# Performance work log

Measured on AMD Instinct MI355X. Metric: run time of the kernel, lower is better.

The kernel has to match this reference:

```python
import jax, jax.numpy as jnp
import numpy as np

B, S, H = 32, 2048, 1024
UNITS = 1024


def setup_inputs() -> dict:
    key = jax.random.key(0)
    ks = jax.random.split(key, 8)
    scale_h = 1.0 / np.sqrt(H)
    scale_u = 1.0 / np.sqrt(UNITS)
    return {
        "query": jax.random.normal(ks[0], (B, H), dtype=jnp.float32),
        "values": jax.random.normal(ks[1], (B, S, H), dtype=jnp.float32),
        "W1": jax.random.normal(ks[2], (H, UNITS), dtype=jnp.float32) * scale_h,
        "b1": jnp.zeros((UNITS,), dtype=jnp.float32),
        "W2": jax.random.normal(ks[3], (H, UNITS), dtype=jnp.float32) * scale_h,
        "b2": jnp.zeros((UNITS,), dtype=jnp.float32),
        "V": jax.random.normal(ks[4], (UNITS, 1), dtype=jnp.float32) * scale_u,
        "bv": jnp.zeros((1,), dtype=jnp.float32),
    }


def reference(query, values, W1, b1, W2, b2, V, bv):
    # proj_v: [B, S, units]; proj_q: [B, 1, units] (query expanded on time axis)
    proj_v = jnp.einsum("bsh,hu->bsu", values, W1) + b1
    proj_q = (query @ W2 + b2)[:, None, :]
    # score: [B, S, 1]
    score = jnp.tanh(proj_v + proj_q) @ V + bv
    attention_weights = jax.nn.softmax(score, axis=1)  # softmax over seq axis
    context_vector = jnp.sum(attention_weights * values, axis=1)  # [B, H]
    return context_vector, attention_weights
```

## Files before the change

### kernel.cpp

```cpp
#include <hip/hip_runtime.h>

#define H 1024
#define UNITS 1024
#define BATCH 32
#define SEQ 2048
#define M_TOT (BATCH * SEQ)

typedef __attribute__((ext_vector_type(8))) short bf16x8;
typedef __attribute__((ext_vector_type(8))) unsigned short u16x8;
typedef __attribute__((ext_vector_type(4))) float f32x4;

__device__ __forceinline__ unsigned short f2bf(float f) {
  union { float f; unsigned u; } x; x.f = f;
  unsigned r = x.u + 0x7FFFu + ((x.u >> 16) & 1u);
  return (unsigned short)(r >> 16);
}
__device__ __forceinline__ float bf2f(unsigned short h) {
  union { unsigned u; float f; } x; x.u = (unsigned)h << 16;
  return x.f;
}

__device__ __forceinline__ void gll16(const unsigned short* g, unsigned short* l) {
  __builtin_amdgcn_global_load_lds(
      (const __attribute__((address_space(1))) void*)g,
      (__attribute__((address_space(3))) void*)l, 16, 0, 0);
}

__global__ void k_cast(const float* __restrict__ in, unsigned short* __restrict__ out) {
  size_t i = ((size_t)blockIdx.x * 256 + threadIdx.x) * 8;
  float4 v0 = *reinterpret_cast<const float4*>(in + i);
  float4 v1 = *reinterpret_cast<const float4*>(in + i + 4);
  union { unsigned short h[8]; u16x8 v; } p;
  p.h[0] = f2bf(v0.x); p.h[1] = f2bf(v0.y); p.h[2] = f2bf(v0.z); p.h[3] = f2bf(v0.w);
  p.h[4] = f2bf(v1.x); p.h[5] = f2bf(v1.y); p.h[6] = f2bf(v1.z); p.h[7] = f2bf(v1.w);
  *reinterpret_cast<u16x8*>(out + i) = p.v;
}

__global__ void k_transpose_w1(const float* __restrict__ W1, unsigned short* __restrict__ W1T) {
  __shared__ float tile[32][33];
  int bx = blockIdx.x, by = blockIdx.y;
  int tx = threadIdx.x, ty = threadIdx.y;
#pragma unroll
  for (int i = 0; i < 4; ++i)
    tile[ty + i * 8][tx] = W1[(by * 32 + ty + i * 8) * UNITS + bx * 32 + tx];
  __syncthreads();
#pragma unroll
  for (int i = 0; i < 4; ++i)
    W1T[(bx * 32 + ty + i * 8) * H + by * 32 + tx] = f2bf(tile[tx][ty + i * 8]);
}

__global__ void k_projq(const float* __restrict__ query, const float* __restrict__ W2,
                        const float* __restrict__ b2, float* __restrict__ projq) {
  __shared__ float q[H];
  int b = blockIdx.x;
  int u = blockIdx.y * 256 + threadIdx.x;
  for (int i = threadIdx.x; i < H; i += 256) q[i] = query[b * H + i];
  __syncthreads();
  float acc = 0.f;
#pragma unroll 8
  for (int k = 0; k < H; ++k) acc = fmaf(q[k], W2[k * UNITS + u], acc);
  projq[b * UNITS + u] = acc + b2[u];
}

#define BM 256
#define BN 256
#define NKT 32

__global__ __launch_bounds__(512, 2) void k_score3(
    const unsigned short* __restrict__ Vb,
    const unsigned short* __restrict__ W1T,
    const float* __restrict__ b1,
    const float* __restrict__ projq,
    const float* __restrict__ V,
    float* __restrict__ scores)
{
  __shared__ unsigned short As[4][128][64];
  __shared__ unsigned short Bs[4][128][64];

  const int tid = threadIdx.x;
  const int lane = tid & 63;
  const int wave = tid >> 6;
  const int wm = wave >> 2;
  const int wn = wave & 3;
  const int li = lane & 15, hi = lane >> 4;
  const int lr2 = li >> 1;
  const int pcol = (((((li & 1) << 2) + hi) ^ lr2) & 7) << 3;

  const int g = blockIdx.x;
  const int xcd = g & 7;
  const int local = g >> 3;
  const int n_t = local & 3;
  const int m_t = xcd + ((local >> 2) << 3);
  const int m0 = m_t * BM;
  const int n0 = n_t * BN;

  const int sL = (lane & 7) ^ (lane >> 3);
  const int srow = 2 * (lane >> 3) + (sL >> 2);
  const int scol = (sL & 3) << 3;

  auto STAGE_A = [&](int bf, int kt) {
#pragma unroll
    for (int q = 0; q < 2; ++q) {
      int mb = wave * 32 + q * 16;
      gll16(&Vb[(size_t)(m0 + mb + srow) * H + kt * 32 + scol],
            &As[bf][wave * 16 + q * 8][0]);
    }
  };
  auto STAGE_B = [&](int bf, int kt) {
#pragma unroll
    for (int q = 0; q < 2; ++q) {
      int mb = wave * 32 + q * 16;
      gll16(&W1T[(size_t)(n0 + mb + srow) * H + kt * 32 + scol],
            &Bs[bf][wave * 16 + q * 8][0]);
    }
  };

  f32x4 acc[8][4] = {};

  STAGE_A(0, 0); STAGE_B(0, 0);
  STAGE_A(1, 1); STAGE_B(1, 1);
  STAGE_A(2, 2); STAGE_B(2, 2);

#pragma unroll 4
  for (int c = 0; c < NKT; ++c) {
    const int buf = c & 3;
    const int nbuf = (c + 3) & 3;
    const int cn = (c < NKT - 3) ? c + 3 : NKT - 1;

    asm volatile("s_waitcnt vmcnt(8)" ::: "memory");
    __builtin_amdgcn_s_barrier();

    bf16x8 a[8], b[4];
#pragma unroll
    for (int i = 0; i < 8; ++i)
      a[i] = *reinterpret_cast<const bf16x8*>(&As[buf][wm * 64 + i * 8 + lr2][pcol]);
    STAGE_A(nbuf, cn);
#pragma unroll
    for (int j = 0; j < 4; ++j)
      b[j] = *reinterpret_cast<const bf16x8*>(&Bs[buf][wn * 32 + j * 8 + lr2][pcol]);
    STAGE_B(nbuf, cn);

    __builtin_amdgcn_s_setprio(1);
#pragma unroll
    for (int i = 0; i < 8; ++i)
#pragma unroll
      for (int j = 0; j < 4; ++j)
        acc[i][j] = __builtin_amdgcn_mfma_f32_16x16x32_bf16(a[i], b[j], acc[i][j], 0, 0, 0);
    __builtin_amdgcn_s_setprio(0);
  }

  const int b = m0 >> 11;
  float bias[4], vv[4];
#pragma unroll
  for (int j = 0; j < 4; ++j) {
    int u = n0 + wn * 64 + j * 16 + li;
    bias[j] = b1[u] + projq[b * UNITS + u];
    vv[j] = V[u];
  }
#pragma unroll
  for (int mi = 0; mi < 8; ++mi) {
#pragma unroll
    for (int r = 0; r < 4; ++r) {
      float s = 0.f;
#pragma unroll
      for (int j = 0; j < 4; ++j) {
        float x = acc[mi][j][r] + bias[j];
        float e = __expf(2.f * x);
        s += (1.f - 2.f / (e + 1.f)) * vv[j];
      }
      s += __shfl_xor(s, 1);
      s += __shfl_xor(s, 2);
      s += __shfl_xor(s, 4);
      s += __shfl_xor(s, 8);
      if (li == 0) {
        int row = m0 + wm * 128 + mi * 16 + hi * 4 + r;
        atomicAdd(&scores[row], s);
      }
    }
  }
}

#define FBM 128
#define FBN 128
#define FBK 64
#define LDK 72
__global__ __launch_bounds__(256) void k_score_f32(
    const float* __restrict__ values, const unsigned short* __restrict__ W1T,
    const float* __restrict__ b1, const float* __restrict__ projq,
    const float* __restrict__ V, float* __restrict__ scores)
{
  __shared__ unsigned short Asf[FBM][LDK];
  __shared__ unsigned short Bsf[FBN][LDK];
  const int tid = threadIdx.x;
  const int lane = tid & 63;
  const int wave = tid >> 6;
  const int wm = wave >> 1, wn = wave & 1;
  const int li = lane & 15, hi = lane >> 4;
  const int n0 = blockIdx.x * FBN;
  const int m0 = blockIdx.y * FBM;
  f32x4 acc[4][4] = {};
  for (int k0 = 0; k0 < H; k0 += FBK) {
    __syncthreads();
#pragma unroll
    for (int q = 0; q < 8; ++q) {
      int idx = q * 256 + tid;
      int row = idx >> 4;
      int kc = (idx & 15) << 2;
      float4 v = *reinterpret_cast<const float4*>(&values[(size_t)(m0 + row) * H + k0 + kc]);
      union { unsigned short h[4]; unsigned long long u64; } p;
      p.h[0] = f2bf(v.x); p.h[1] = f2bf(v.y); p.h[2] = f2bf(v.z); p.h[3] = f2bf(v.w);
      *reinterpret_cast<unsigned long long*>(&Asf[row][kc]) = p.u64;
    }
#pragma unroll
    for (int q = 0; q < 4; ++q) {
      int idx = q * 256 + tid;
      int row = idx >> 3;
      int kc = (idx & 7) << 3;
      *reinterpret_cast<u16x8*>(&Bsf[row][kc]) =
          *reinterpret_cast<const u16x8*>(&W1T[(size_t)(n0 + row) * H + k0 + kc]);
    }
    __syncthreads();
#pragma unroll
    for (int ks = 0; ks < 2; ++ks) {
      const int kofs = ks * 32 + 8 * hi;
      bf16x8 a[4], bb[4];
#pragma unroll
      for (int i = 0; i < 4; ++i)
        a[i] = *reinterpret_cast<const bf16x8*>(&Asf[wm * 64 + i * 16 + li][kofs]);
#pragma unroll
      for (int i = 0; i < 4; ++i)
        bb[i] = *reinterpret_cast<const bf16x8*>(&Bsf[wn * 64 + i * 16 + li][kofs]);
#pragma unroll
      for (int mi = 0; mi < 4; ++mi)
#pragma unroll
        for (int ni = 0; ni < 4; ++ni)
          acc[mi][ni] = __builtin_amdgcn_mfma_f32_16x16x32_bf16(a[mi], bb[ni], acc[mi][ni], 0, 0, 0);
    }
  }
  const int b = m0 >> 11;
  float bias[4], vv[4];
#pragma unroll
  for (int ni = 0; ni < 4; ++ni) {
    int u = n0 + wn * 64 + ni * 16 + li;
    bias[ni] = b1[u] + projq[b * UNITS + u];
    vv[ni] = V[u];
  }
#pragma unroll
  for (int mi = 0; mi < 4; ++mi) {
#pragma unroll
    for (int r = 0; r < 4; ++r) {
      float s = 0.f;
#pragma unroll
      for (int ni = 0; ni < 4; ++ni) {
        float x = acc[mi][ni][r] + bias[ni];
        float e = __expf(2.f * x);
        s += (1.f - 2.f / (e + 1.f)) * vv[ni];
      }
      s += __shfl_xor(s, 1);
      s += __shfl_xor(s, 2);
      s += __shfl_xor(s, 4);
      s += __shfl_xor(s, 8);
      if (li == 0) atomicAdd(&scores[m0 + wm * 64 + mi * 16 + hi * 4 + r], s);
    }
  }
}

__global__ void k_softmax(const float* __restrict__ scores, float* __restrict__ wts) {
  __shared__ float red[8];
  int b = blockIdx.x;
  int t = threadIdx.x;
  float v[8];
  float mx = -3.4e38f;
#pragma unroll
  for (int i = 0; i < 8; ++i) {
    v[i] = scores[b * SEQ + i * 256 + t];
    mx = fmaxf(mx, v[i]);
  }
#pragma unroll
  for (int o = 1; o < 64; o <<= 1) mx = fmaxf(mx, __shfl_xor(mx, o));
  if ((t & 63) == 0) red[t >> 6] = mx;
  __syncthreads();
  mx = fmaxf(fmaxf(red[0], red[1]), fmaxf(red[2], red[3]));
  float sum = 0.f;
#pragma unroll
  for (int i = 0; i < 8; ++i) { v[i] = __expf(v[i] - mx); sum += v[i]; }
#pragma unroll
  for (int o = 1; o < 64; o <<= 1) sum += __shfl_xor(sum, o);
  if ((t & 63) == 0) red[4 + (t >> 6)] = sum;
  __syncthreads();
  float inv = 1.f / (red[4] + red[5] + red[6] + red[7]);
#pragma unroll
  for (int i = 0; i < 8; ++i) wts[b * SEQ + i * 256 + t] = v[i] * inv;
}

__global__ void k_context_bf(const unsigned short* __restrict__ Vb,
                             const float* __restrict__ wts, float* __restrict__ ctx) {
  int b = blockIdx.x, sc = blockIdx.y;
  int h4 = threadIdx.x * 4;
  const unsigned short* vb = Vb + (size_t)b * SEQ * H;
  float a0 = 0, a1 = 0, a2 = 0, a3 = 0;
  int s0 = sc * 128;
#pragma unroll 4
  for (int s = s0; s < s0 + 128; ++s) {
    float w = wts[b * SEQ + s];
    ushort4 v = *reinterpret_cast<const ushort4*>(&vb[(size_t)s * H + h4]);
    a0 = fmaf(w, bf2f(v.x), a0);
    a1 = fmaf(w, bf2f(v.y), a1);
    a2 = fmaf(w, bf2f(v.z), a2);
    a3 = fmaf(w, bf2f(v.w), a3);
  }
  atomicAdd(&ctx[b * H + h4 + 0], a0);
  atomicAdd(&ctx[b * H + h4 + 1], a1);
  atomicAdd(&ctx[b * H + h4 + 2], a2);
  atomicAdd(&ctx[b * H + h4 + 3], a3);
}

__global__ void k_context(const float* __restrict__ values, const float* __restrict__ wts,
                          float* __restrict__ ctx) {
  int b = blockIdx.x, hc = blockIdx.y, sc = blockIdx.z;
  int h = hc * 256 + threadIdx.x;
  const float* vb = values + (size_t)b * SEQ * H;
  float acc = 0.f;
  int s0 = sc * 128;
#pragma unroll 4
  for (int s = s0; s < s0 + 128; ++s)
    acc = fmaf(wts[b * SEQ + s], vb[(size_t)s * H + h], acc);
  atomicAdd(&ctx[b * H + h], acc);
}

extern "C" void kernel_launch(void* const* d_in, const int* in_sizes, int n_in,
                              void* d_out, int out_size, void* d_ws, size_t ws_size,
                              hipStream_t stream) {
  (void)in_sizes; (void)n_in; (void)out_size;
  const float* query  = (const float*)d_in[0];
  const float* values = (const float*)d_in[1];
  const float* W1     = (const float*)d_in[2];
  const float* b1     = (const float*)d_in[3];
  const float* W2     = (const float*)d_in[4];
  const float* b2     = (const float*)d_in[5];
  const float* V      = (const float*)d_in[6];

  float* out = (float*)d_out;
  float* ctx = out;
  float* wts = out + BATCH * H;

  const size_t vb_bytes = (size_t)M_TOT * H * 2;
  const size_t need = vb_bytes + (2u << 20) + (256u << 10) + (128u << 10);

  if (ws_size >= need) {
    char* ws = (char*)d_ws;
    unsigned short* Vb  = (unsigned short*)ws;
    unsigned short* W1T = (unsigned short*)(ws + vb_bytes);
    float* scores = (float*)(ws + vb_bytes + (2u << 20));
    float* projq  = (float*)(ws + vb_bytes + (2u << 20) + (256u << 10));

    hipMemsetAsync(scores, 0, M_TOT * sizeof(float), stream);
    hipMemsetAsync(ctx, 0, BATCH * H * sizeof(float), stream);

    k_cast<<<(M_TOT * H / 8) / 256, 256, 0, stream>>>(values, Vb);
    k_transpose_w1<<<dim3(32, 32), dim3(32, 8), 0, stream>>>(W1, W1T);
    k_projq<<<dim3(32, 4), 256, 0, stream>>>(query, W2, b2, projq);
    k_score3<<<(M_TOT / BM) * (UNITS / BN), 512, 0, stream>>>(Vb, W1T, b1, projq, V, scores);
    k_softmax<<<BATCH, 256, 0, stream>>>(scores, wts);
    k_context_bf<<<dim3(BATCH, 16), 256, 0, stream>>>(Vb, wts, ctx);
  } else {
    char* ws = (char*)d_ws;
    unsigned short* W1T = (unsigned short*)ws;
    float* scores = (float*)(ws + (2u << 20));
    float* projq  = (float*)(ws + (2u << 20) + (256u << 10));

    hipMemsetAsync(scores, 0, M_TOT * sizeof(float), stream);
    hipMemsetAsync(ctx, 0, BATCH * H * sizeof(float), stream);

    k_transpose_w1<<<dim3(32, 32), dim3(32, 8), 0, stream>>>(W1, W1T);
    k_projq<<<dim3(32, 4), 256, 0, stream>>>(query, W2, b2, projq);
    k_score_f32<<<dim3(UNITS / FBN, M_TOT / FBM), 256, 0, stream>>>(values, W1T, b1, projq, V, scores);
    k_softmax<<<BATCH, 256, 0, stream>>>(scores, wts);
    k_context<<<dim3(BATCH, H / 256, 16), 256, 0, stream>>>(values, wts, ctx);
  }
}
```

Baseline: 328.2 us.

## Shrink score GEMM tile to 256x128 with 4 waves and triple-buffered staging

Reshapes the main projection-score GEMM from a 256x256 tile on 8 waves to a 256x128 tile on 4 waves. Each wave keeps the same 128x64 output footprint. The LDS pipeline drops from four buffers with prefetch distance 3 to three buffers with distance 2. Loads for the next stage are now issued right after the barrier, and an explicit LDS wait plus sched_barrier is placed before the MFMA block. The aim is to reduce LDS use and improve occupancy and scheduling, at the cost of reloading the A operand (values) twice as often and a shallower prefetch.

```diff
diff --git a/kernel.cpp b/kernel.cpp
--- a/kernel.cpp
+++ b/kernel.cpp
@@ -63,10 +63,10 @@
 }
 
 #define BM 256
-#define BN 256
+#define BN 128
 #define NKT 32
 
-__global__ __launch_bounds__(512, 2) void k_score3(
+__global__ __launch_bounds__(256, 2) void k_score5(
     const unsigned short* __restrict__ Vb,
     const unsigned short* __restrict__ W1T,
     const float* __restrict__ b1,
@@ -74,14 +74,14 @@
     const float* __restrict__ V,
     float* __restrict__ scores)
 {
-  __shared__ unsigned short As[4][128][64];
-  __shared__ unsigned short Bs[4][128][64];
+  __shared__ unsigned short As[3][128][64];
+  __shared__ unsigned short Bs[3][64][64];
 
   const int tid = threadIdx.x;
   const int lane = tid & 63;
   const int wave = tid >> 6;
-  const int wm = wave >> 2;
-  const int wn = wave & 3;
+  const int wm = wave >> 1;
+  const int wn = wave & 1;
   const int li = lane & 15, hi = lane >> 4;
   const int lr2 = li >> 1;
   const int pcol = (((((li & 1) << 2) + hi) ^ lr2) & 7) << 3;
@@ -89,8 +89,8 @@
   const int g = blockIdx.x;
   const int xcd = g & 7;
   const int local = g >> 3;
-  const int n_t = local & 3;
-  const int m_t = xcd + ((local >> 2) << 3);
+  const int n_t = local & 7;
+  const int m_t = xcd + ((local >> 3) << 3);
   const int m0 = m_t * BM;
   const int n0 = n_t * BN;
 
@@ -98,48 +98,47 @@
   const int srow = 2 * (lane >> 3) + (sL >> 2);
   const int scol = (sL & 3) << 3;
 
-  auto STAGE_A = [&](int bf, int kt) {
+  auto STAGE = [&](int bf, int kt) {
+#pragma unroll
+    for (int q = 0; q < 4; ++q) {
+      int ch = wave * 4 + q;
+      gll16(&Vb[(size_t)(m0 + ch * 16 + srow) * H + kt * 32 + scol],
+            &As[bf][ch * 8][0]);
+    }
 #pragma unroll
     for (int q = 0; q < 2; ++q) {
-      int mb = wave * 32 + q * 16;
-      gll16(&Vb[(size_t)(m0 + mb + srow) * H + kt * 32 + scol],
-            &As[bf][wave * 16 + q * 8][0]);
+      int ch = wave * 2 + q;
+      gll16(&W1T[(size_t)(n0 + ch * 16 + srow) * H + kt * 32 + scol],
+            &Bs[bf][ch * 8][0]);
     }
   };
-  auto STAGE_B = [&](int bf, int kt) {
-#pragma unroll
-    for (int q = 0; q < 2; ++q) {
-      int mb = wave * 32 + q * 16;
-      gll16(&W1T[(size_t)(n0 + mb + srow) * H + kt * 32 + scol],
-            &Bs[bf][wave * 16 + q * 8][0]);
-    }
-  };
 
   f32x4 acc[8][4] = {};
 
-  STAGE_A(0, 0); STAGE_B(0, 0);
-  STAGE_A(1, 1); STAGE_B(1, 1);
-  STAGE_A(2, 2); STAGE_B(2, 2);
-
-#pragma unroll 4
+  STAGE(0, 0);
+  STAGE(1, 1);
+
+#pragma unroll 2
   for (int c = 0; c < NKT; ++c) {
-    const int buf = c & 3;
-    const int nbuf = (c + 3) & 3;
-    const int cn = (c < NKT - 3) ? c + 3 : NKT - 1;
-
-    asm volatile("s_waitcnt vmcnt(8)" ::: "memory");
+    const int buf = c % 3;
+    const int nbuf = (c + 2) % 3;
+    const int cn = (c + 2 < NKT) ? c + 2 : NKT - 1;
+
+    asm volatile("s_waitcnt vmcnt(6)" ::: "memory");
     __builtin_amdgcn_s_barrier();
+
+    STAGE(nbuf, cn);
 
     bf16x8 a[8], b[4];
 #pragma unroll
     for (int i = 0; i < 8; ++i)
       a[i] = *reinterpret_cast<const bf16x8*>(&As[buf][wm * 64 + i * 8 + lr2][pcol]);
-    STAGE_A(nbuf, cn);
 #pragma unroll
     for (int j = 0; j < 4; ++j)
       b[j] = *reinterpret_cast<const bf16x8*>(&Bs[buf][wn * 32 + j * 8 + lr2][pcol]);
-    STAGE_B(nbuf, cn);
-
+
+    asm volatile("s_waitcnt lgkmcnt(0)" ::: "memory");
+    __builtin_amdgcn_sched_barrier(0);
     __builtin_amdgcn_s_setprio(1);
 #pragma unroll
     for (int i = 0; i < 8; ++i)
@@ -360,7 +359,7 @@
     k_cast<<<(M_TOT * H / 8) / 256, 256, 0, stream>>>(values, Vb);
     k_transpose_w1<<<dim3(32, 32), dim3(32, 8), 0, stream>>>(W1, W1T);
     k_projq<<<dim3(32, 4), 256, 0, stream>>>(query, W2, b2, projq);
-    k_score3<<<(M_TOT / BM) * (UNITS / BN), 512, 0, stream>>>(Vb, W1T, b1, projq, V, scores);
+    k_score5<<<(M_TOT / BM) * (UNITS / BN), 256, 0, stream>>>(Vb, W1T, b1, projq, V, scores);
     k_softmax<<<BATCH, 256, 0, stream>>>(scores, wts);
     k_context_bf<<<dim3(BATCH, 16), 256, 0, stream>>>(Vb, wts, ctx);
   } else {
```

Measured after the change: 345.7 us. 5.3% more time.
